# Kernel tuning notes

Measured on AMD Instinct MI355X. Metric: run time of the kernel, lower is better.

Reference implementation:

```python
import jax, jax.numpy as jnp
import numpy as np

CH = 512
NUM_GROUPS = 32
EPS = 1e-6

def _xavier(key, shape):
    fan_in, fan_out = shape[1], shape[0]
    limit = np.sqrt(6.0 / (fan_in + fan_out))
    return jax.random.uniform(key, shape, jnp.float32, -limit, limit)

def setup_inputs() -> dict:
    key = jax.random.key(0)
    ks = jax.random.split(key, 6)
    B, C, H, W = 32, CH, 32, 32
    x = jax.random.normal(ks[0], (B, C, H, W), jnp.float32)
    # 1x1 conv weights stored as [C_out, C_in]; biases zero (per initialize())
    wq = _xavier(ks[1], (C, C)); wk = _xavier(ks[2], (C, C))
    wv = _xavier(ks[3], (C, C)); wp = _xavier(ks[4], (C, C))
    bq = jnp.zeros((C,)); bk = jnp.zeros((C,)); bv = jnp.zeros((C,)); bp = jnp.zeros((C,))
    gn_w = jnp.ones((C,)); gn_b = jnp.zeros((C,))
    return {"x": x, "gn_w": gn_w, "gn_b": gn_b,
            "wq": wq, "bq": bq, "wk": wk, "bk": bk,
            "wv": wv, "bv": bv, "wp": wp, "bp": bp}

def _group_norm(x, w, b):
    B, C, H, W = x.shape
    g = NUM_GROUPS
    xg = x.reshape(B, g, C // g, H, W)
    mean = xg.mean(axis=(2, 3, 4), keepdims=True)
    var = xg.var(axis=(2, 3, 4), keepdims=True)
    xn = ((xg - mean) * jax.lax.rsqrt(var + EPS)).reshape(B, C, H, W)
    return xn * w[None, :, None, None] + b[None, :, None, None]

def reference(x, gn_w, gn_b, wq, bq, wk, bk, wv, bv, wp, bp):
    B, C, H, W = x.shape
    h = _group_norm(x, gn_w, gn_b)
    hf = h.reshape(B, C, H * W)  # [B, C, N]
    # 1x1 convs == per-pixel linear over channels
    q = jnp.einsum('oc,bcn->bno', wq, hf) + bq  # [B, N, C]
    k = jnp.einsum('oc,bcn->bon', wk, hf) + bk[None, :, None]  # [B, C, N]
    v = jnp.einsum('oc,bcn->bno', wv, hf) + bv  # [B, N, C]
    attn = jnp.einsum('bqc,bck->bqk', q, k) * (C ** -0.5)  # [B, N, N]
    attn = jax.nn.softmax(attn, axis=-1)
    out = jnp.einsum('bqk,bkc->bqc', attn, v)  # [B, N, C]
    out = jnp.einsum('oc,bnc->bon', wp, out) + bp[None, :, None]  # [B, C, N]
    return x + out.reshape(B, C, H, W)
```

## Files before the change

kernel.cpp:

```cpp
#include <hip/hip_runtime.h>


#define C_DIM 512
#define N_PIX 1024
#define BATCH 32
#define CPG 16
#define EPS 1e-6f
#define SCALE 0.044194173824159216f
#define ESTRIDE 66
#define ESTRU   72

typedef unsigned short u16;
typedef __attribute__((ext_vector_type(8))) short bf16x8;
typedef __attribute__((ext_vector_type(4))) float f32x4;
typedef __attribute__((ext_vector_type(2))) float f32x2;

static __device__ __forceinline__ float bf2f(u16 u) {
    union { unsigned int i; float f; } v; v.i = ((unsigned int)u) << 16; return v.f;
}
static __device__ __forceinline__ u16 f2bf(float f) {
    union { float f; unsigned int i; } v; v.f = f;
    unsigned int r = v.i + 0x7fffu + ((v.i >> 16) & 1u);
    return (u16)(r >> 16);
}

static __device__ __forceinline__ void gl_lds16(const u16* g, u16* l) {
    __builtin_amdgcn_global_load_lds(
        (const __attribute__((address_space(1))) unsigned int*)g,
        (__attribute__((address_space(3))) unsigned int*)l,
        16, 0, 0);
}

#define BAR()   __builtin_amdgcn_s_barrier()
#define SCHED() __builtin_amdgcn_sched_barrier(0x7)

__global__ __launch_bounds__(256) void wconv_kernel(
        const float* __restrict__ wq, const float* __restrict__ wk,
        const float* __restrict__ wv, const float* __restrict__ wp,
        u16* __restrict__ out) {
    int i = blockIdx.x * 256 + threadIdx.x;
    int mat = i >> 16;
    const float* src = (mat == 0) ? wq : (mat == 1) ? wk : (mat == 2) ? wv : wp;
    float4 v = ((const float4*)src)[i & 65535];
    ushort4 o;
    o.x = f2bf(v.x); o.y = f2bf(v.y); o.z = f2bf(v.z); o.w = f2bf(v.w);
    *(ushort4*)&out[(size_t)i * 4] = o;
}

__global__ __launch_bounds__(256) void gn_kernel(
        const float* __restrict__ x, const float* __restrict__ gw,
        const float* __restrict__ gb, u16* __restrict__ h) {
    int blk = blockIdx.x;
    int b = blk >> 5, g = blk & 31;
    size_t base = ((size_t)(b * C_DIM + g * CPG)) * N_PIX;
    const float4* xv = (const float4*)(x + base);
    int tid = threadIdx.x;

    float s = 0.f, sq = 0.f;
    for (int i = tid; i < (CPG * N_PIX) / 4; i += 256) {
        float4 v = xv[i];
        s  += v.x + v.y + v.z + v.w;
        sq += v.x * v.x + v.y * v.y + v.z * v.z + v.w * v.w;
    }
    __shared__ float rs[256], rq[256];
    rs[tid] = s; rq[tid] = sq;
    __syncthreads();
    for (int off = 128; off > 0; off >>= 1) {
        if (tid < off) { rs[tid] += rs[tid + off]; rq[tid] += rq[tid + off]; }
        __syncthreads();
    }
    float mean = rs[0] * (1.0f / (CPG * N_PIX));
    float var  = rq[0] * (1.0f / (CPG * N_PIX)) - mean * mean;
    float inv  = rsqrtf(var + EPS);

    __shared__ u16 Ls[CPG * N_PIX];
    for (int i = tid; i < (CPG * N_PIX) / 4; i += 256) {
        int c_local = i >> 8;
        int c = g * CPG + c_local;
        float sc = gw[c] * inv;
        float sh = gb[c] - mean * sc;
        float4 v = xv[i];
        ushort4 o;
        o.x = f2bf(v.x * sc + sh); o.y = f2bf(v.y * sc + sh);
        o.z = f2bf(v.z * sc + sh); o.w = f2bf(v.w * sc + sh);
        *(ushort4*)&Ls[c_local * N_PIX + (i & 255) * 4] = o;
    }
    __syncthreads();
    u16* hb = h + (size_t)b * N_PIX * C_DIM + g * CPG;
    for (int n = tid; n < N_PIX; n += 256) {
        unsigned int pk[8];
#pragma unroll
        for (int j = 0; j < 8; ++j) {
            unsigned int lo = Ls[(2 * j) * N_PIX + n];
            unsigned int hi = Ls[(2 * j + 1) * N_PIX + n];
            pk[j] = lo | (hi << 16);
        }
        uint4* dst = (uint4*)(hb + (size_t)n * C_DIM);
        dst[0] = make_uint4(pk[0], pk[1], pk[2], pk[3]);
        dst[1] = make_uint4(pk[4], pk[5], pk[6], pk[7]);
    }
}


#define MM(mq, nq) do { \
    _Pragma("unroll") \
    for (int t_ = 0; t_ < 4; ++t_) { \
        _Pragma("unroll") \
        for (int n_ = 0; n_ < 2; ++n_) { \
            _Pragma("unroll") \
            for (int ks_ = 0; ks_ < 2; ++ks_) \
                acc[(mq)*4 + t_][(nq)*2 + n_] = \
                    __builtin_amdgcn_mfma_f32_16x16x32_bf16( \
                        af[t_][ks_], bf[(nq)*2 + n_][ks_], \
                        acc[(mq)*4 + t_][(nq)*2 + n_], 0, 0, 0); \
        } \
    } \
} while (0)

template <int MODE>
__global__ __launch_bounds__(512, 2) void gemm_kernel(
        const u16* __restrict__ A, const u16* __restrict__ A2,
        const u16* __restrict__ B, const u16* __restrict__ B2,
        void* __restrict__ Cv, void* __restrict__ Cv2,
        const float* __restrict__ bias, const float* __restrict__ bias2,
        const float* __restrict__ xres, int K,
        int rsA, int rsB, int rsC,
        long long bsA, long long bsB, long long bsC) {
    int nx = gridDim.x, ny = gridDim.y;
    int nwg = nx * ny * gridDim.z;
    int flat = blockIdx.x + nx * (blockIdx.y + ny * blockIdx.z);
    int t = (flat & 7) * (nwg >> 3) + (flat >> 3);
    int bx = t % nx, by = (t / nx) % ny, bz = t / (nx * ny);

    int mat = 0, b = bz;
    const u16 *gA, *gB;
    void* out = Cv;
    const float* bi_p = bias;
    if (MODE == 0) {
        mat = bz & 1; b = bz >> 1;
        gA = A + (size_t)b * bsA + (size_t)by * 256 * rsA;
        gB = B + (size_t)mat * 262144 + (size_t)bx * 256 * rsB;
        out = mat ? Cv2 : Cv;
        bi_p = mat ? bias2 : bias;
    } else if (MODE == 2) {
        gA = A + (size_t)b * bsA + (size_t)by * 256 * rsA;
        gB = B + (size_t)b * bsB + (size_t)bx * 256 * rsB;
        out = (b >= 16) ? Cv2 : Cv;
    } else if (MODE == 3) {
        gA = ((b >= 16) ? A2 : A) + (size_t)(b & 15) * bsA + (size_t)by * 256 * rsA;
        gB = B + (size_t)b * bsB + (size_t)bx * 256 * rsB;
        out = (b >= 16) ? Cv2 : Cv;
    } else if (MODE == 4) {
        gA = A + (size_t)by * 256 * rsA;
        gB = ((b >= 16) ? B2 : B) + (size_t)(b & 15) * bsB + (size_t)bx * 256 * rsB;
    } else {
        gA = A + (size_t)by * 256 * rsA;
        gB = B + (size_t)b * bsB + (size_t)bx * 256 * rsB;
    }
    int cb = (MODE == 2 || MODE == 3) ? (b & 15) : b;

    __shared__ __align__(16) u16 smem[65536];

    int tid = threadIdx.x;
    int lane = tid & 63, wave = tid >> 6;
    int wm = wave >> 2, wn = wave & 3;
    int quad = lane >> 4, l15 = lane & 15, l7 = lane & 7;
    int srow = tid >> 3;
    int lg = (tid & 7) ^ (srow & 7);

    const int nk = K >> 6;
    const int nit = nk >> 1;

    auto STG = [&](int buf, int isB, int h, int kt) {
        const u16* g = isB ? gB : gA;
        int rs = isB ? rsB : rsA;
        const u16* src = g + (size_t)(h * 128 + srow) * rs + (size_t)kt * 64 + lg * 8;
        u16* dst = &smem[buf * 32768 + isB * 16384 + (h * 128 + srow) * 64 + (tid & 7) * 8];
        gl_lds16(src, dst);
        gl_lds16(src + (size_t)64 * rs, dst + 4096);
    };
    auto LDA = [&](int buf, int mq, int t_, int ks) -> bf16x8 {
        return *(const bf16x8*)&smem[buf * 32768 +
            (wm * 128 + mq * 64 + t_ * 16 + l15) * 64 + (((ks * 4 + quad) ^ l7) << 3)];
    };
    auto LDB = [&](int buf, int nt, int ks) -> bf16x8 {
        return *(const bf16x8*)&smem[buf * 32768 + 16384 +
            (wn * 64 + nt * 16 + l15) * 64 + (((ks * 4 + quad) ^ l7) << 3)];
    };

    f32x4 acc[8][4];
#pragma unroll
    for (int mt = 0; mt < 8; ++mt)
#pragma unroll
        for (int nt = 0; nt < 4; ++nt)
            acc[mt][nt] = (f32x4){0.f, 0.f, 0.f, 0.f};
    bf16x8 af[4][2], bf[4][2];

    STG(0, 1, 0, 0); STG(0, 1, 1, 0);
    STG(0, 0, 0, 0); STG(0, 0, 1, 0);
    STG(1, 1, 0, 1); STG(1, 1, 1, 1);
    asm volatile("s_waitcnt vmcnt(4)" ::: "memory");
    SCHED(); BAR(); SCHED();

    for (int it = 0; it < nit; ++it) {
        const bool s = (it + 1 < nit);
        const int k1 = 2 * it + 1, k2 = 2 * it + 2, k3 = 2 * it + 3;

#pragma unroll
        for (int t_ = 0; t_ < 4; ++t_)
#pragma unroll
            for (int ks = 0; ks < 2; ++ks) af[t_][ks] = LDA(0, 0, t_, ks);
#pragma unroll
        for (int n = 0; n < 2; ++n)
#pragma unroll
            for (int ks = 0; ks < 2; ++ks) bf[n][ks] = LDB(0, n, ks);
        STG(1, 0, 0, k1);
        SCHED(); BAR(); SCHED();
        __builtin_amdgcn_s_setprio(1); MM(0, 0); __builtin_amdgcn_s_setprio(0);
        SCHED(); BAR(); SCHED();

#pragma unroll
        for (int n = 2; n < 4; ++n)
#pragma unroll
            for (int ks = 0; ks < 2; ++ks) bf[n][ks] = LDB(0, n, ks);
        STG(1, 0, 1, k1);
        SCHED(); BAR(); SCHED();
        __builtin_amdgcn_s_setprio(1); MM(0, 1); __builtin_amdgcn_s_setprio(0);
        SCHED(); BAR(); SCHED();

#pragma unroll
        for (int t_ = 0; t_ < 4; ++t_)
#pragma unroll
            for (int ks = 0; ks < 2; ++ks) af[t_][ks] = LDA(0, 1, t_, ks);
        if (s) STG(0, 1, 0, k2);
        SCHED(); BAR(); SCHED();
        __builtin_amdgcn_s_setprio(1); MM(1, 1); __builtin_amdgcn_s_setprio(0);
        SCHED(); BAR(); SCHED();

        if (s) STG(0, 1, 1, k2);
        SCHED(); BAR(); SCHED();
        __builtin_amdgcn_s_setprio(1); MM(1, 0); __builtin_amdgcn_s_setprio(0);
        if (s) asm volatile("s_waitcnt vmcnt(4)" ::: "memory");
        else   asm volatile("s_waitcnt vmcnt(0)" ::: "memory");
        SCHED(); BAR(); SCHED();

#pragma unroll
        for (int t_ = 0; t_ < 4; ++t_)
#pragma unroll
            for (int ks = 0; ks < 2; ++ks) af[t_][ks] = LDA(1, 0, t_, ks);
#pragma unroll
        for (int n = 0; n < 2; ++n)
#pragma unroll
            for (int ks = 0; ks < 2; ++ks) bf[n][ks] = LDB(1, n, ks);
        if (s) STG(0, 0, 0, k2);
        SCHED(); BAR(); SCHED();
        __builtin_amdgcn_s_setprio(1); MM(0, 0); __builtin_amdgcn_s_setprio(0);
        SCHED(); BAR(); SCHED();

#pragma unroll
        for (int n = 2; n < 4; ++n)
#pragma unroll
            for (int ks = 0; ks < 2; ++ks) bf[n][ks] = LDB(1, n, ks);
        if (s) STG(0, 0, 1, k2);
        SCHED(); BAR(); SCHED();
        __builtin_amdgcn_s_setprio(1); MM(0, 1); __builtin_amdgcn_s_setprio(0);
        SCHED(); BAR(); SCHED();

#pragma unroll
        for (int t_ = 0; t_ < 4; ++t_)
#pragma unroll
            for (int ks = 0; ks < 2; ++ks) af[t_][ks] = LDA(1, 1, t_, ks);
        if (s) STG(1, 1, 0, k3);
        SCHED(); BAR(); SCHED();
        __builtin_amdgcn_s_setprio(1); MM(1, 1); __builtin_amdgcn_s_setprio(0);
        SCHED(); BAR(); SCHED();

        if (s) STG(1, 1, 1, k3);
        SCHED(); BAR(); SCHED();
        __builtin_amdgcn_s_setprio(1); MM(1, 0); __builtin_amdgcn_s_setprio(0);
        if (s) asm volatile("s_waitcnt vmcnt(4)" ::: "memory");
        SCHED(); BAR(); SCHED();
    }

    int colb = bx * 256 + wn * 64;
    int rowb = by * 256 + wm * 128;

    if (MODE == 4) {
        float* ebw = (float*)smem + wave * (16 * ESTRIDE);
        int er = lane >> 4;
        int ec4 = (lane & 15) * 4;
#pragma unroll
        for (int mt = 0; mt < 8; ++mt) {
#pragma unroll
            for (int nt = 0; nt < 4; ++nt) {
                f32x4 a = acc[mt][nt];
#pragma unroll
                for (int reg = 0; reg < 4; ++reg)
                    ebw[(quad * 4 + reg) * ESTRIDE + nt * 16 + l15] = a[reg];
            }
#pragma unroll
            for (int j = 0; j < 4; ++j) {
                int lr = er + 4 * j;
                f32x2 v0 = *(f32x2*)&ebw[lr * ESTRIDE + ec4];
                f32x2 v1 = *(f32x2*)&ebw[lr * ESTRIDE + ec4 + 2];
                int gr = rowb + mt * 16 + lr;
                int gc = colb + ec4;
                size_t cidx = (size_t)cb * bsC + (size_t)gr * rsC + gc;
                float bi = bi_p[gr];
                float4 xr = *(const float4*)&xres[cidx];
                float4 st = make_float4(v0.x + bi + xr.x, v0.y + bi + xr.y,
                                        v1.x + bi + xr.z, v1.y + bi + xr.w);
                *(float4*)&((float*)out)[cidx] = st;
            }
        }
    } else {
        u16* ebw = (u16*)smem + wave * (16 * ESTRU);
        int er = lane >> 3;
        int ec = (lane & 7) * 8;
        float bcol[4];
        if (MODE == 0) {
#pragma unroll
            for (int nt = 0; nt < 4; ++nt)
                bcol[nt] = bi_p[colb + nt * 16 + l15];
        }
#pragma unroll
        for (int mt = 0; mt < 8; ++mt) {
            float4 brow;
            if (MODE == 1)
                brow = *(const float4*)&bi_p[rowb + mt * 16 + quad * 4];
#pragma unroll
            for (int nt = 0; nt < 4; ++nt) {
                f32x4 a = acc[mt][nt];
#pragma unroll
                for (int reg = 0; reg < 4; ++reg) {
                    float fv = a[reg];
                    if (MODE == 0) fv += bcol[nt];
                    else if (MODE == 1) fv += ((const float*)&brow)[reg];
                    else if (MODE == 2) fv *= SCALE;
                    ebw[(quad * 4 + reg) * ESTRU + nt * 16 + l15] = f2bf(fv);
                }
            }
#pragma unroll
            for (int j = 0; j < 2; ++j) {
                int lr = er + 8 * j;
                bf16x8 vv = *(const bf16x8*)&ebw[lr * ESTRU + ec];
                int gr = rowb + mt * 16 + lr;
                size_t cidx = (size_t)cb * bsC + (size_t)gr * rsC + colb + ec;
                *(bf16x8*)&((u16*)out)[cidx] = vv;
            }
        }
    }
}

__global__ __launch_bounds__(256) void softmax_kernel(
        u16* __restrict__ S0, u16* __restrict__ S1) {
    int row = blockIdx.x;
    u16* base = (row & 16384) ? S1 : S0;
    u16* p = base + (size_t)(row & 16383) * N_PIX;
    int tid = threadIdx.x;
    ushort4 uv = *(ushort4*)&p[tid * 4];
    float4 v = make_float4(bf2f(uv.x), bf2f(uv.y), bf2f(uv.z), bf2f(uv.w));
    __shared__ float red[256];
    float m = fmaxf(fmaxf(v.x, v.y), fmaxf(v.z, v.w));
    red[tid] = m; __syncthreads();
    for (int off = 128; off > 0; off >>= 1) {
        if (tid < off) red[tid] = fmaxf(red[tid], red[tid + off]);
        __syncthreads();
    }
    float M = red[0];
    __syncthreads();
    float4 e;
    e.x = __expf(v.x - M); e.y = __expf(v.y - M);
    e.z = __expf(v.z - M); e.w = __expf(v.w - M);
    red[tid] = e.x + e.y + e.z + e.w; __syncthreads();
    for (int off = 128; off > 0; off >>= 1) {
        if (tid < off) red[tid] += red[tid + off];
        __syncthreads();
    }
    float inv = 1.0f / red[0];
    ushort4 st;
    st.x = f2bf(e.x * inv); st.y = f2bf(e.y * inv);
    st.z = f2bf(e.z * inv); st.w = f2bf(e.w * inv);
    *(ushort4*)&p[tid * 4] = st;
}

extern "C" void kernel_launch(void* const* d_in, const int* in_sizes, int n_in,
                              void* d_out, int out_size, void* d_ws, size_t ws_size,
                              hipStream_t stream) {
    const float* x    = (const float*)d_in[0];
    const float* gn_w = (const float*)d_in[1];
    const float* gn_b = (const float*)d_in[2];
    const float* wq   = (const float*)d_in[3];
    const float* bq   = (const float*)d_in[4];
    const float* wk   = (const float*)d_in[5];
    const float* bk   = (const float*)d_in[6];
    const float* wv   = (const float*)d_in[7];
    const float* bv   = (const float*)d_in[8];
    const float* wp   = (const float*)d_in[9];
    const float* bp   = (const float*)d_in[10];
    float* y = (float*)d_out;

    const size_t BCN = (size_t)BATCH * C_DIM * N_PIX;
    char* w = (char*)d_ws;
    u16* h  = (u16*)(w);
    u16* q  = (u16*)(w + 2 * BCN);
    u16* k  = (u16*)(w + 4 * BCN);
    u16* v  = (u16*)(w + 6 * BCN);
    u16* Or = (u16*)(w + 8 * BCN);
    u16* wb = (u16*)(w + 10 * BCN);
    u16* wvb = wb + 524288, *wpb = wb + 786432;
    u16* S0 = h;
    u16* S1 = Or;
    u16* O0 = q;
    u16* O1 = k;

    const long long BS = 524288;
    const long long SB = 1048576;

    wconv_kernel<<<1024, 256, 0, stream>>>(wq, wk, wv, wp, wb);
    gn_kernel<<<1024, 256, 0, stream>>>(x, gn_w, gn_b, h);

    gemm_kernel<0><<<dim3(2, 4, 64), 512, 0, stream>>>(
        h, nullptr, wb, nullptr, q, k, bq, bk, nullptr,
        512, 512, 512, 512, BS, 0, BS);
    gemm_kernel<1><<<dim3(4, 2, 32), 512, 0, stream>>>(
        wvb, nullptr, h, nullptr, v, nullptr, bv, nullptr, nullptr,
        512, 512, 512, 1024, 0, BS, BS);

    gemm_kernel<2><<<dim3(4, 4, 32), 512, 0, stream>>>(
        q, nullptr, k, nullptr, S0, S1, nullptr, nullptr, nullptr,
        512, 512, 512, 1024, BS, BS, SB);
    softmax_kernel<<<32 * 1024, 256, 0, stream>>>(S0, S1);
    gemm_kernel<3><<<dim3(2, 4, 32), 512, 0, stream>>>(
        S0, S1, v, nullptr, O0, O1, nullptr, nullptr, nullptr,
        1024, 1024, 1024, 512, SB, BS, BS);

    gemm_kernel<4><<<dim3(4, 2, 32), 512, 0, stream>>>(
        wpb, nullptr, O0, O1, y, nullptr, bp, nullptr, x,
        512, 512, 512, 1024, 0, BS, BS);
}
```

Measured before the change: 359.0 us.

## Persistent multi-tile GEMM with cross-tile prefetch, split groupnorm, warp-level softmax

```diff
diff --git a/kernel.cpp b/kernel.cpp
--- a/kernel.cpp
+++ b/kernel.cpp
@@ -34,70 +34,90 @@
 #define BAR()   __builtin_amdgcn_s_barrier()
 #define SCHED() __builtin_amdgcn_sched_barrier(0x7)
 
-__global__ __launch_bounds__(256) void wconv_kernel(
+__global__ __launch_bounds__(256) void prep_kernel(
         const float* __restrict__ wq, const float* __restrict__ wk,
         const float* __restrict__ wv, const float* __restrict__ wp,
-        u16* __restrict__ out) {
-    int i = blockIdx.x * 256 + threadIdx.x;
-    int mat = i >> 16;
-    const float* src = (mat == 0) ? wq : (mat == 1) ? wk : (mat == 2) ? wv : wp;
-    float4 v = ((const float4*)src)[i & 65535];
-    ushort4 o;
-    o.x = f2bf(v.x); o.y = f2bf(v.y); o.z = f2bf(v.z); o.w = f2bf(v.w);
-    *(ushort4*)&out[(size_t)i * 4] = o;
-}
-
-__global__ __launch_bounds__(256) void gn_kernel(
-        const float* __restrict__ x, const float* __restrict__ gw,
-        const float* __restrict__ gb, u16* __restrict__ h) {
+        u16* __restrict__ out, const float* __restrict__ x,
+        float* __restrict__ stats) {
     int blk = blockIdx.x;
+    if (blk < 1024) {
+        int i = blk * 256 + threadIdx.x;
+        int mat = i >> 16;
+        const float* src = (mat == 0) ? wq : (mat == 1) ? wk : (mat == 2) ? wv : wp;
+        float4 v = ((const float4*)src)[i & 65535];
+        ushort4 o;
+        o.x = f2bf(v.x); o.y = f2bf(v.y); o.z = f2bf(v.z); o.w = f2bf(v.w);
+        *(ushort4*)&out[(size_t)i * 4] = o;
+        return;
+    }
+    blk -= 1024;
     int b = blk >> 5, g = blk & 31;
-    size_t base = ((size_t)(b * C_DIM + g * CPG)) * N_PIX;
-    const float4* xv = (const float4*)(x + base);
+    const float4* xv = (const float4*)(x + ((size_t)(b * C_DIM + g * CPG)) * N_PIX);
     int tid = threadIdx.x;
-
     float s = 0.f, sq = 0.f;
+#pragma unroll 4
     for (int i = tid; i < (CPG * N_PIX) / 4; i += 256) {
         float4 v = xv[i];
         s  += v.x + v.y + v.z + v.w;
         sq += v.x * v.x + v.y * v.y + v.z * v.z + v.w * v.w;
     }
-    __shared__ float rs[256], rq[256];
-    rs[tid] = s; rq[tid] = sq;
+#pragma unroll
+    for (int m = 1; m < 64; m <<= 1) {
+        s += __shfl_xor(s, m);
+        sq += __shfl_xor(sq, m);
+    }
+    __shared__ float rs[4], rq[4];
+    int wv_ = tid >> 6;
+    if ((tid & 63) == 0) { rs[wv_] = s; rq[wv_] = sq; }
     __syncthreads();
-    for (int off = 128; off > 0; off >>= 1) {
-        if (tid < off) { rs[tid] += rs[tid + off]; rq[tid] += rq[tid + off]; }
-        __syncthreads();
-    }
-    float mean = rs[0] * (1.0f / (CPG * N_PIX));
-    float var  = rq[0] * (1.0f / (CPG * N_PIX)) - mean * mean;
-    float inv  = rsqrtf(var + EPS);
-
-    __shared__ u16 Ls[CPG * N_PIX];
-    for (int i = tid; i < (CPG * N_PIX) / 4; i += 256) {
-        int c_local = i >> 8;
-        int c = g * CPG + c_local;
+    if (tid == 0) {
+        float S = rs[0] + rs[1] + rs[2] + rs[3];
+        float Q = rq[0] + rq[1] + rq[2] + rq[3];
+        float mean = S * (1.0f / (CPG * N_PIX));
+        float var  = Q * (1.0f / (CPG * N_PIX)) - mean * mean;
+        stats[blk * 2] = mean;
+        stats[blk * 2 + 1] = rsqrtf(var + EPS);
+    }
+}
+
+__global__ __launch_bounds__(256) void gnt_kernel(
+        const float* __restrict__ x, const float* __restrict__ gw,
+        const float* __restrict__ gb, const float* __restrict__ stats,
+        u16* __restrict__ h) {
+    int blk = blockIdx.x;
+    int b = blk >> 4, nc = blk & 15;
+    int n0 = nc * 64;
+    __shared__ u16 T[64 * 520];
+    int tid = threadIdx.x;
+    int cq = tid >> 4;
+    int n4 = tid & 15;
+    const float* xb = x + (size_t)b * C_DIM * N_PIX + n0;
+#pragma unroll 4
+    for (int pass = 0; pass < 32; ++pass) {
+        int c = pass * 16 + cq;
+        int g = c >> 4;
+        float mean = stats[(b * 32 + g) * 2];
+        float inv  = stats[(b * 32 + g) * 2 + 1];
         float sc = gw[c] * inv;
         float sh = gb[c] - mean * sc;
-        float4 v = xv[i];
-        ushort4 o;
-        o.x = f2bf(v.x * sc + sh); o.y = f2bf(v.y * sc + sh);
-        o.z = f2bf(v.z * sc + sh); o.w = f2bf(v.w * sc + sh);
-        *(ushort4*)&Ls[c_local * N_PIX + (i & 255) * 4] = o;
+        float4 v = *(const float4*)(xb + (size_t)c * N_PIX + n4 * 4);
+        int nn = n4 * 4;
+        T[(nn + 0) * 520 + c] = f2bf(v.x * sc + sh);
+        T[(nn + 1) * 520 + c] = f2bf(v.y * sc + sh);
+        T[(nn + 2) * 520 + c] = f2bf(v.z * sc + sh);
+        T[(nn + 3) * 520 + c] = f2bf(v.w * sc + sh);
     }
     __syncthreads();
-    u16* hb = h + (size_t)b * N_PIX * C_DIM + g * CPG;
-    for (int n = tid; n < N_PIX; n += 256) {
-        unsigned int pk[8];
-#pragma unroll
-        for (int j = 0; j < 8; ++j) {
-            unsigned int lo = Ls[(2 * j) * N_PIX + n];
-            unsigned int hi = Ls[(2 * j + 1) * N_PIX + n];
-            pk[j] = lo | (hi << 16);
-        }
-        uint4* dst = (uint4*)(hb + (size_t)n * C_DIM);
-        dst[0] = make_uint4(pk[0], pk[1], pk[2], pk[3]);
-        dst[1] = make_uint4(pk[4], pk[5], pk[6], pk[7]);
+    u16* hb = h + ((size_t)b * N_PIX + n0) * C_DIM;
+    int rr = tid >> 5;
+    int cc = (tid & 31) * 16;
+#pragma unroll
+    for (int p = 0; p < 8; ++p) {
+        int n = p * 8 + rr;
+        bf16x8 v0 = *(const bf16x8*)&T[n * 520 + cc];
+        bf16x8 v1 = *(const bf16x8*)&T[n * 520 + cc + 8];
+        *(bf16x8*)&hb[(size_t)n * C_DIM + cc] = v0;
+        *(bf16x8*)&hb[(size_t)n * C_DIM + cc + 8] = v1;
     }
 }
 
@@ -117,7 +137,7 @@
     } \
 } while (0)
 
-template <int MODE>
+template <int MODE, int NT>
 __global__ __launch_bounds__(512, 2) void gemm_kernel(
         const u16* __restrict__ A, const u16* __restrict__ A2,
         const u16* __restrict__ B, const u16* __restrict__ B2,
@@ -125,39 +145,47 @@
         const float* __restrict__ bias, const float* __restrict__ bias2,
         const float* __restrict__ xres, int K,
         int rsA, int rsB, int rsC,
-        long long bsA, long long bsB, long long bsC) {
-    int nx = gridDim.x, ny = gridDim.y;
-    int nwg = nx * ny * gridDim.z;
-    int flat = blockIdx.x + nx * (blockIdx.y + ny * blockIdx.z);
-    int t = (flat & 7) * (nwg >> 3) + (flat >> 3);
-    int bx = t % nx, by = (t / nx) % ny, bz = t / (nx * ny);
-
-    int mat = 0, b = bz;
-    const u16 *gA, *gB;
-    void* out = Cv;
-    const float* bi_p = bias;
-    if (MODE == 0) {
-        mat = bz & 1; b = bz >> 1;
-        gA = A + (size_t)b * bsA + (size_t)by * 256 * rsA;
-        gB = B + (size_t)mat * 262144 + (size_t)bx * 256 * rsB;
-        out = mat ? Cv2 : Cv;
-        bi_p = mat ? bias2 : bias;
-    } else if (MODE == 2) {
-        gA = A + (size_t)b * bsA + (size_t)by * 256 * rsA;
-        gB = B + (size_t)b * bsB + (size_t)bx * 256 * rsB;
-        out = (b >= 16) ? Cv2 : Cv;
-    } else if (MODE == 3) {
-        gA = ((b >= 16) ? A2 : A) + (size_t)(b & 15) * bsA + (size_t)by * 256 * rsA;
-        gB = B + (size_t)b * bsB + (size_t)bx * 256 * rsB;
-        out = (b >= 16) ? Cv2 : Cv;
-    } else if (MODE == 4) {
-        gA = A + (size_t)by * 256 * rsA;
-        gB = ((b >= 16) ? B2 : B) + (size_t)(b & 15) * bsB + (size_t)bx * 256 * rsB;
-    } else {
-        gA = A + (size_t)by * 256 * rsA;
-        gB = B + (size_t)b * bsB + (size_t)bx * 256 * rsB;
-    }
-    int cb = (MODE == 2 || MODE == 3) ? (b & 15) : b;
+        long long bsA, long long bsB, long long bsC,
+        int nx, int ny) {
+    const int nwg = 256 * NT;
+
+    const u16* tgA[2]; const u16* tgB[2];
+    void* tout[2]; const float* tbi[2];
+    int tcb[2], tcolb[2], trowb[2];
+#pragma unroll
+    for (int tt = 0; tt < NT; ++tt) {
+        int flat = blockIdx.x + tt * 256;
+        int t = (flat & 7) * (nwg >> 3) + (flat >> 3);
+        int bx = t % nx, by = (t / nx) % ny, bz = t / (nx * ny);
+        int b = bz;
+        const u16 *gA, *gB;
+        void* out = Cv;
+        const float* bi = bias;
+        if (MODE == 0) {
+            int mat = bz & 1; b = bz >> 1;
+            gA = A + (size_t)b * bsA + (size_t)by * 256 * rsA;
+            gB = B + (size_t)mat * 262144 + (size_t)bx * 256 * rsB;
+            out = mat ? Cv2 : Cv;
+            bi = mat ? bias2 : bias;
+        } else if (MODE == 2) {
+            gA = A + (size_t)b * bsA + (size_t)by * 256 * rsA;
+            gB = B + (size_t)b * bsB + (size_t)bx * 256 * rsB;
+            out = (b >= 16) ? Cv2 : Cv;
+        } else if (MODE == 3) {
+            gA = ((b >= 16) ? A2 : A) + (size_t)(b & 15) * bsA + (size_t)by * 256 * rsA;
+            gB = B + (size_t)b * bsB + (size_t)bx * 256 * rsB;
+            out = (b >= 16) ? Cv2 : Cv;
+        } else if (MODE == 4) {
+            gA = A + (size_t)by * 256 * rsA;
+            gB = ((b >= 16) ? B2 : B) + (size_t)(b & 15) * bsB + (size_t)bx * 256 * rsB;
+        } else {
+            gA = A + (size_t)by * 256 * rsA;
+            gB = B + (size_t)b * bsB + (size_t)bx * 256 * rsB;
+        }
+        tgA[tt] = gA; tgB[tt] = gB; tout[tt] = out; tbi[tt] = bi;
+        tcb[tt] = (MODE == 2 || MODE == 3) ? (b & 15) : b;
+        tcolb[tt] = bx * 256; trowb[tt] = by * 256;
+    }
 
     __shared__ __align__(16) u16 smem[65536];
 
@@ -171,11 +199,9 @@
     const int nk = K >> 6;
     const int nit = nk >> 1;
 
-    auto STG = [&](int buf, int isB, int h, int kt) {
-        const u16* g = isB ? gB : gA;
-        int rs = isB ? rsB : rsA;
-        const u16* src = g + (size_t)(h * 128 + srow) * rs + (size_t)kt * 64 + lg * 8;
-        u16* dst = &smem[buf * 32768 + isB * 16384 + (h * 128 + srow) * 64 + (tid & 7) * 8];
+    auto STG = [&](const u16* g, int rs, int buf, int isB, int hh, int kt) {
+        const u16* src = g + (size_t)(hh * 128 + srow) * rs + (size_t)kt * 64 + lg * 8;
+        u16* dst = &smem[buf * 32768 + isB * 16384 + (hh * 128 + srow) * 64 + (tid & 7) * 8];
         gl_lds16(src, dst);
         gl_lds16(src + (size_t)64 * rs, dst + 4096);
     };
@@ -189,199 +215,228 @@
     };
 
     f32x4 acc[8][4];
-#pragma unroll
-    for (int mt = 0; mt < 8; ++mt)
-#pragma unroll
-        for (int nt = 0; nt < 4; ++nt)
-            acc[mt][nt] = (f32x4){0.f, 0.f, 0.f, 0.f};
     bf16x8 af[4][2], bf[4][2];
 
-    STG(0, 1, 0, 0); STG(0, 1, 1, 0);
-    STG(0, 0, 0, 0); STG(0, 0, 1, 0);
-    STG(1, 1, 0, 1); STG(1, 1, 1, 1);
-    asm volatile("s_waitcnt vmcnt(4)" ::: "memory");
-    SCHED(); BAR(); SCHED();
-
-    for (int it = 0; it < nit; ++it) {
-        const bool s = (it + 1 < nit);
-        const int k1 = 2 * it + 1, k2 = 2 * it + 2, k3 = 2 * it + 3;
-
-#pragma unroll
-        for (int t_ = 0; t_ < 4; ++t_)
-#pragma unroll
-            for (int ks = 0; ks < 2; ++ks) af[t_][ks] = LDA(0, 0, t_, ks);
-#pragma unroll
-        for (int n = 0; n < 2; ++n)
-#pragma unroll
-            for (int ks = 0; ks < 2; ++ks) bf[n][ks] = LDB(0, n, ks);
-        STG(1, 0, 0, k1);
-        SCHED(); BAR(); SCHED();
-        __builtin_amdgcn_s_setprio(1); MM(0, 0); __builtin_amdgcn_s_setprio(0);
-        SCHED(); BAR(); SCHED();
-
-#pragma unroll
-        for (int n = 2; n < 4; ++n)
-#pragma unroll
-            for (int ks = 0; ks < 2; ++ks) bf[n][ks] = LDB(0, n, ks);
-        STG(1, 0, 1, k1);
-        SCHED(); BAR(); SCHED();
-        __builtin_amdgcn_s_setprio(1); MM(0, 1); __builtin_amdgcn_s_setprio(0);
-        SCHED(); BAR(); SCHED();
-
-#pragma unroll
-        for (int t_ = 0; t_ < 4; ++t_)
-#pragma unroll
-            for (int ks = 0; ks < 2; ++ks) af[t_][ks] = LDA(0, 1, t_, ks);
-        if (s) STG(0, 1, 0, k2);
-        SCHED(); BAR(); SCHED();
-        __builtin_amdgcn_s_setprio(1); MM(1, 1); __builtin_amdgcn_s_setprio(0);
-        SCHED(); BAR(); SCHED();
-
-        if (s) STG(0, 1, 1, k2);
-        SCHED(); BAR(); SCHED();
-        __builtin_amdgcn_s_setprio(1); MM(1, 0); __builtin_amdgcn_s_setprio(0);
-        if (s) asm volatile("s_waitcnt vmcnt(4)" ::: "memory");
-        else   asm volatile("s_waitcnt vmcnt(0)" ::: "memory");
-        SCHED(); BAR(); SCHED();
-
-#pragma unroll
-        for (int t_ = 0; t_ < 4; ++t_)
-#pragma unroll
-            for (int ks = 0; ks < 2; ++ks) af[t_][ks] = LDA(1, 0, t_, ks);
-#pragma unroll
-        for (int n = 0; n < 2; ++n)
-#pragma unroll
-            for (int ks = 0; ks < 2; ++ks) bf[n][ks] = LDB(1, n, ks);
-        if (s) STG(0, 0, 0, k2);
-        SCHED(); BAR(); SCHED();
-        __builtin_amdgcn_s_setprio(1); MM(0, 0); __builtin_amdgcn_s_setprio(0);
-        SCHED(); BAR(); SCHED();
-
-#pragma unroll
-        for (int n = 2; n < 4; ++n)
-#pragma unroll
-            for (int ks = 0; ks < 2; ++ks) bf[n][ks] = LDB(1, n, ks);
-        if (s) STG(0, 0, 1, k2);
-        SCHED(); BAR(); SCHED();
-        __builtin_amdgcn_s_setprio(1); MM(0, 1); __builtin_amdgcn_s_setprio(0);
-        SCHED(); BAR(); SCHED();
-
-#pragma unroll
-        for (int t_ = 0; t_ < 4; ++t_)
-#pragma unroll
-            for (int ks = 0; ks < 2; ++ks) af[t_][ks] = LDA(1, 1, t_, ks);
-        if (s) STG(1, 1, 0, k3);
-        SCHED(); BAR(); SCHED();
-        __builtin_amdgcn_s_setprio(1); MM(1, 1); __builtin_amdgcn_s_setprio(0);
-        SCHED(); BAR(); SCHED();
-
-        if (s) STG(1, 1, 1, k3);
-        SCHED(); BAR(); SCHED();
-        __builtin_amdgcn_s_setprio(1); MM(1, 0); __builtin_amdgcn_s_setprio(0);
-        if (s) asm volatile("s_waitcnt vmcnt(4)" ::: "memory");
-        SCHED(); BAR(); SCHED();
-    }
-
-    int colb = bx * 256 + wn * 64;
-    int rowb = by * 256 + wm * 128;
-
-    if (MODE == 4) {
-        float* ebw = (float*)smem + wave * (16 * ESTRIDE);
-        int er = lane >> 4;
-        int ec4 = (lane & 15) * 4;
-#pragma unroll
-        for (int mt = 0; mt < 8; ++mt) {
-#pragma unroll
-            for (int nt = 0; nt < 4; ++nt) {
-                f32x4 a = acc[mt][nt];
-#pragma unroll
-                for (int reg = 0; reg < 4; ++reg)
-                    ebw[(quad * 4 + reg) * ESTRIDE + nt * 16 + l15] = a[reg];
+#pragma unroll
+    for (int tt = 0; tt < NT; ++tt) {
+        const bool hn = (tt + 1 < NT);
+        const u16* cA = tgA[tt];
+        const u16* cB = tgB[tt];
+        const u16* nA = tgA[hn ? tt + 1 : tt];
+        const u16* nB = tgB[hn ? tt + 1 : tt];
+
+        if (tt == 0) {
+            STG(cB, rsB, 0, 1, 0, 0); STG(cB, rsB, 0, 1, 1, 0);
+            STG(cA, rsA, 0, 0, 0, 0); STG(cA, rsA, 0, 0, 1, 0);
+            STG(cB, rsB, 1, 1, 0, 1); STG(cB, rsB, 1, 1, 1, 1);
+            asm volatile("s_waitcnt vmcnt(4)" ::: "memory");
+            SCHED(); BAR(); SCHED();
+        }
+
+#pragma unroll
+        for (int mt = 0; mt < 8; ++mt)
+#pragma unroll
+            for (int nt = 0; nt < 4; ++nt)
+                acc[mt][nt] = (f32x4){0.f, 0.f, 0.f, 0.f};
+
+        for (int it = 0; it < nit; ++it) {
+            const bool s = (it + 1 < nit);
+            const int k1 = 2 * it + 1, k2 = 2 * it + 2, k3 = 2 * it + 3;
+
+#pragma unroll
+            for (int t_ = 0; t_ < 4; ++t_)
+#pragma unroll
+                for (int ks = 0; ks < 2; ++ks) af[t_][ks] = LDA(0, 0, t_, ks);
+#pragma unroll
+            for (int n = 0; n < 2; ++n)
+#pragma unroll
+                for (int ks = 0; ks < 2; ++ks) bf[n][ks] = LDB(0, n, ks);
+            STG(cA, rsA, 1, 0, 0, k1);
+            SCHED(); BAR(); SCHED();
+            __builtin_amdgcn_s_setprio(1); MM(0, 0); __builtin_amdgcn_s_setprio(0);
+            SCHED(); BAR(); SCHED();
+
+#pragma unroll
+            for (int n = 2; n < 4; ++n)
+#pragma unroll
+                for (int ks = 0; ks < 2; ++ks) bf[n][ks] = LDB(0, n, ks);
+            STG(cA, rsA, 1, 0, 1, k1);
+            SCHED(); BAR(); SCHED();
+            __builtin_amdgcn_s_setprio(1); MM(0, 1); __builtin_amdgcn_s_setprio(0);
+            SCHED(); BAR(); SCHED();
+
+#pragma unroll
+            for (int t_ = 0; t_ < 4; ++t_)
+#pragma unroll
+                for (int ks = 0; ks < 2; ++ks) af[t_][ks] = LDA(0, 1, t_, ks);
+            if (s) STG(cB, rsB, 0, 1, 0, k2);
+            else if (hn) STG(nB, rsB, 0, 1, 0, 0);
+            SCHED(); BAR(); SCHED();
+            __builtin_amdgcn_s_setprio(1); MM(1, 1); __builtin_amdgcn_s_setprio(0);
+            SCHED(); BAR(); SCHED();
+
+            if (s) STG(cB, rsB, 0, 1, 1, k2);
+            else if (hn) STG(nB, rsB, 0, 1, 1, 0);
+            SCHED(); BAR(); SCHED();
+            __builtin_amdgcn_s_setprio(1); MM(1, 0); __builtin_amdgcn_s_setprio(0);
+            if (s || hn) asm volatile("s_waitcnt vmcnt(4)" ::: "memory");
+            else         asm volatile("s_waitcnt vmcnt(0)" ::: "memory");
+            SCHED(); BAR(); SCHED();
+
+#pragma unroll
+            for (int t_ = 0; t_ < 4; ++t_)
+#pragma unroll
+                for (int ks = 0; ks < 2; ++ks) af[t_][ks] = LDA(1, 0, t_, ks);
+#pragma unroll
+            for (int n = 0; n < 2; ++n)
+#pragma unroll
+                for (int ks = 0; ks < 2; ++ks) bf[n][ks] = LDB(1, n, ks);
+            if (s) STG(cA, rsA, 0, 0, 0, k2);
+            else if (hn) STG(nA, rsA, 0, 0, 0, 0);
+            SCHED(); BAR(); SCHED();
+            __builtin_amdgcn_s_setprio(1); MM(0, 0); __builtin_amdgcn_s_setprio(0);
+            SCHED(); BAR(); SCHED();
+
+#pragma unroll
+            for (int n = 2; n < 4; ++n)
+#pragma unroll
+                for (int ks = 0; ks < 2; ++ks) bf[n][ks] = LDB(1, n, ks);
+            if (s) STG(cA, rsA, 0, 0, 1, k2);
+            else if (hn) STG(nA, rsA, 0, 0, 1, 0);
+            SCHED(); BAR(); SCHED();
+            __builtin_amdgcn_s_setprio(1); MM(0, 1); __builtin_amdgcn_s_setprio(0);
+            SCHED(); BAR(); SCHED();
+
+#pragma unroll
+            for (int t_ = 0; t_ < 4; ++t_)
+#pragma unroll
+                for (int ks = 0; ks < 2; ++ks) af[t_][ks] = LDA(1, 1, t_, ks);
+            if (s) STG(cB, rsB, 1, 1, 0, k3);
+            else if (hn) STG(nB, rsB, 1, 1, 0, 1);
+            SCHED(); BAR(); SCHED();
+            __builtin_amdgcn_s_setprio(1); MM(1, 1); __builtin_amdgcn_s_setprio(0);
+            SCHED(); BAR(); SCHED();
+
+            if (s) STG(cB, rsB, 1, 1, 1, k3);
+            else if (hn) STG(nB, rsB, 1, 1, 1, 1);
+            SCHED(); BAR(); SCHED();
+            __builtin_amdgcn_s_setprio(1); MM(1, 0); __builtin_amdgcn_s_setprio(0);
+            if (s) asm volatile("s_waitcnt vmcnt(4)" ::: "memory");
+            SCHED(); BAR(); SCHED();
+        }
+
+        int colb = tcolb[tt] + wn * 64;
+        int rowb = trowb[tt] + wm * 128;
+        void* out = tout[tt];
+        const float* bi_p = tbi[tt];
+        int cb = tcb[tt];
+
+        if (MODE == 4) {
+            float* ebw = (float*)(smem + 32768) + wave * (16 * ESTRIDE);
+            int er = lane >> 4;
+            int ec4 = (lane & 15) * 4;
+#pragma unroll
+            for (int mt = 0; mt < 8; ++mt) {
+#pragma unroll
+                for (int nt = 0; nt < 4; ++nt) {
+                    f32x4 a = acc[mt][nt];
+#pragma unroll
+                    for (int reg = 0; reg < 4; ++reg)
+                        ebw[(quad * 4 + reg) * ESTRIDE + nt * 16 + l15] = a[reg];
+                }
+#pragma unroll
+                for (int j = 0; j < 4; ++j) {
+                    int lr = er + 4 * j;
+                    f32x2 v0 = *(f32x2*)&ebw[lr * ESTRIDE + ec4];
+                    f32x2 v1 = *(f32x2*)&ebw[lr * ESTRIDE + ec4 + 2];
+                    int gr = rowb + mt * 16 + lr;
+                    int gc = colb + ec4;
+                    size_t cidx = (size_t)cb * bsC + (size_t)gr * rsC + gc;
+                    float bi = bi_p[gr];
+                    float4 xr = *(const float4*)&xres[cidx];
+                    float4 st = make_float4(v0.x + bi + xr.x, v0.y + bi + xr.y,
+                                            v1.x + bi + xr.z, v1.y + bi + xr.w);
+                    *(float4*)&((float*)out)[cidx] = st;
+                }
             }
-#pragma unroll
-            for (int j = 0; j < 4; ++j) {
-                int lr = er + 4 * j;
-                f32x2 v0 = *(f32x2*)&ebw[lr * ESTRIDE + ec4];
-                f32x2 v1 = *(f32x2*)&ebw[lr * ESTRIDE + ec4 + 2];
-                int gr = rowb + mt * 16 + lr;
-                int gc = colb + ec4;
-                size_t cidx = (size_t)cb * bsC + (size_t)gr * rsC + gc;
-                float bi = bi_p[gr];
-                float4 xr = *(const float4*)&xres[cidx];
-                float4 st = make_float4(v0.x + bi + xr.x, v0.y + bi + xr.y,
-                                        v1.x + bi + xr.z, v1.y + bi + xr.w);
-                *(float4*)&((float*)out)[cidx] = st;
+        } else {
+            u16* ebw = (smem + 32768) + wave * (16 * ESTRU);
+            int er = lane >> 3;
+            int ec = (lane & 7) * 8;
+            float bcol[4];
+            if (MODE == 0) {
+#pragma unroll
+                for (int nt = 0; nt < 4; ++nt)
+                    bcol[nt] = bi_p[colb + nt * 16 + l15];
+            }
+#pragma unroll
+            for (int mt = 0; mt < 8; ++mt) {
+                float4 brow;
+                if (MODE == 1)
+                    brow = *(const float4*)&bi_p[rowb + mt * 16 + quad * 4];
+#pragma unroll
+                for (int nt = 0; nt < 4; ++nt) {
+                    f32x4 a = acc[mt][nt];
+#pragma unroll
+                    for (int reg = 0; reg < 4; ++reg) {
+                        float fv = a[reg];
+                        if (MODE == 0) fv += bcol[nt];
+                        else if (MODE == 1) fv += ((const float*)&brow)[reg];
+                        else if (MODE == 2) fv *= SCALE;
+                        ebw[(quad * 4 + reg) * ESTRU + nt * 16 + l15] = f2bf(fv);
+                    }
+                }
+#pragma unroll
+                for (int j = 0; j < 2; ++j) {
+                    int lr = er + 8 * j;
+                    bf16x8 vv = *(const bf16x8*)&ebw[lr * ESTRU + ec];
+                    int gr = rowb + mt * 16 + lr;
+                    size_t cidx = (size_t)cb * bsC + (size_t)gr * rsC + colb + ec;
+                    *(bf16x8*)&((u16*)out)[cidx] = vv;
+                }
             }
         }
-    } else {
-        u16* ebw = (u16*)smem + wave * (16 * ESTRU);
-        int er = lane >> 3;
-        int ec = (lane & 7) * 8;
-        float bcol[4];
-        if (MODE == 0) {
-#pragma unroll
-            for (int nt = 0; nt < 4; ++nt)
-                bcol[nt] = bi_p[colb + nt * 16 + l15];
-        }
-#pragma unroll
-        for (int mt = 0; mt < 8; ++mt) {
-            float4 brow;
-            if (MODE == 1)
-                brow = *(const float4*)&bi_p[rowb + mt * 16 + quad * 4];
-#pragma unroll
-            for (int nt = 0; nt < 4; ++nt) {
-                f32x4 a = acc[mt][nt];
-#pragma unroll
-                for (int reg = 0; reg < 4; ++reg) {
-                    float fv = a[reg];
-                    if (MODE == 0) fv += bcol[nt];
-                    else if (MODE == 1) fv += ((const float*)&brow)[reg];
-                    else if (MODE == 2) fv *= SCALE;
-                    ebw[(quad * 4 + reg) * ESTRU + nt * 16 + l15] = f2bf(fv);
-                }
-            }
-#pragma unroll
-            for (int j = 0; j < 2; ++j) {
-                int lr = er + 8 * j;
-                bf16x8 vv = *(const bf16x8*)&ebw[lr * ESTRU + ec];
-                int gr = rowb + mt * 16 + lr;
-                size_t cidx = (size_t)cb * bsC + (size_t)gr * rsC + colb + ec;
-                *(bf16x8*)&((u16*)out)[cidx] = vv;
-            }
+
+        if (hn) {
+            SCHED();
+            asm volatile("s_waitcnt vmcnt(20)" ::: "memory");
+            BAR(); SCHED();
         }
     }
 }
 
 __global__ __launch_bounds__(256) void softmax_kernel(
         u16* __restrict__ S0, u16* __restrict__ S1) {
-    int row = blockIdx.x;
-    u16* base = (row & 16384) ? S1 : S0;
-    u16* p = base + (size_t)(row & 16383) * N_PIX;
-    int tid = threadIdx.x;
-    ushort4 uv = *(ushort4*)&p[tid * 4];
-    float4 v = make_float4(bf2f(uv.x), bf2f(uv.y), bf2f(uv.z), bf2f(uv.w));
-    __shared__ float red[256];
-    float m = fmaxf(fmaxf(v.x, v.y), fmaxf(v.z, v.w));
-    red[tid] = m; __syncthreads();
-    for (int off = 128; off > 0; off >>= 1) {
-        if (tid < off) red[tid] = fmaxf(red[tid], red[tid + off]);
-        __syncthreads();
-    }
-    float M = red[0];
-    __syncthreads();
-    float4 e;
-    e.x = __expf(v.x - M); e.y = __expf(v.y - M);
-    e.z = __expf(v.z - M); e.w = __expf(v.w - M);
-    red[tid] = e.x + e.y + e.z + e.w; __syncthreads();
-    for (int off = 128; off > 0; off >>= 1) {
-        if (tid < off) red[tid] += red[tid + off];
-        __syncthreads();
-    }
-    float inv = 1.0f / red[0];
-    ushort4 st;
-    st.x = f2bf(e.x * inv); st.y = f2bf(e.y * inv);
-    st.z = f2bf(e.z * inv); st.w = f2bf(e.w * inv);
-    *(ushort4*)&p[tid * 4] = st;
+    int row = blockIdx.x * 4 + (threadIdx.x >> 6);
+    int lane = threadIdx.x & 63;
+    u16* p = ((row & 16384) ? S1 : S0) + (size_t)(row & 16383) * N_PIX + lane * 16;
+    bf16x8 u0 = *(const bf16x8*)p;
+    bf16x8 u1 = *(const bf16x8*)(p + 8);
+    float f[16];
+#pragma unroll
+    for (int i = 0; i < 8; ++i) {
+        f[i] = bf2f((u16)u0[i]);
+        f[8 + i] = bf2f((u16)u1[i]);
+    }
+    float m = f[0];
+#pragma unroll
+    for (int i = 1; i < 16; ++i) m = fmaxf(m, f[i]);
+#pragma unroll
+    for (int off = 1; off < 64; off <<= 1) m = fmaxf(m, __shfl_xor(m, off));
+    float s = 0.f;
+#pragma unroll
+    for (int i = 0; i < 16; ++i) { f[i] = __expf(f[i] - m); s += f[i]; }
+#pragma unroll
+    for (int off = 1; off < 64; off <<= 1) s += __shfl_xor(s, off);
+    float inv = 1.0f / s;
+    bf16x8 s0, s1;
+#pragma unroll
+    for (int i = 0; i < 8; ++i) {
+        s0[i] = (short)f2bf(f[i] * inv);
+        s1[i] = (short)f2bf(f[8 + i] * inv);
+    }
+    *(bf16x8*)p = s0;
+    *(bf16x8*)(p + 8) = s1;
 }
 
 extern "C" void kernel_launch(void* const* d_in, const int* in_sizes, int n_in,
@@ -409,6 +464,7 @@
     u16* Or = (u16*)(w + 8 * BCN);
     u16* wb = (u16*)(w + 10 * BCN);
     u16* wvb = wb + 524288, *wpb = wb + 786432;
+    float* stats = (float*)(w + 10 * BCN + 2 * 1024 * 1024);
     u16* S0 = h;
     u16* S1 = Or;
     u16* O0 = q;
@@ -417,25 +473,25 @@
     const long long BS = 524288;
     const long long SB = 1048576;
 
-    wconv_kernel<<<1024, 256, 0, stream>>>(wq, wk, wv, wp, wb);
-    gn_kernel<<<1024, 256, 0, stream>>>(x, gn_w, gn_b, h);
-
-    gemm_kernel<0><<<dim3(2, 4, 64), 512, 0, stream>>>(
+    prep_kernel<<<2048, 256, 0, stream>>>(wq, wk, wv, wp, wb, x, stats);
+    gnt_kernel<<<512, 256, 0, stream>>>(x, gn_w, gn_b, stats, h);
+
+    gemm_kernel<0, 2><<<256, 512, 0, stream>>>(
         h, nullptr, wb, nullptr, q, k, bq, bk, nullptr,
-        512, 512, 512, 512, BS, 0, BS);
-    gemm_kernel<1><<<dim3(4, 2, 32), 512, 0, stream>>>(
+        512, 512, 512, 512, BS, 0, BS, 2, 4);
+    gemm_kernel<1, 1><<<256, 512, 0, stream>>>(
         wvb, nullptr, h, nullptr, v, nullptr, bv, nullptr, nullptr,
-        512, 512, 512, 1024, 0, BS, BS);
-
-    gemm_kernel<2><<<dim3(4, 4, 32), 512, 0, stream>>>(
+        512, 512, 512, 1024, 0, BS, BS, 4, 2);
+
+    gemm_kernel<2, 2><<<256, 512, 0, stream>>>(
         q, nullptr, k, nullptr, S0, S1, nullptr, nullptr, nullptr,
-        512, 512, 512, 1024, BS, BS, SB);
-    softmax_kernel<<<32 * 1024, 256, 0, stream>>>(S0, S1);
-    gemm_kernel<3><<<dim3(2, 4, 32), 512, 0, stream>>>(
+        512, 512, 512, 1024, BS, BS, SB, 4, 4);
+    softmax_kernel<<<8192, 256, 0, stream>>>(S0, S1);
+    gemm_kernel<3, 1><<<256, 512, 0, stream>>>(
         S0, S1, v, nullptr, O0, O1, nullptr, nullptr, nullptr,
-        1024, 1024, 1024, 512, SB, BS, BS);
-
-    gemm_kernel<4><<<dim3(4, 2, 32), 512, 0, stream>>>(
+        1024, 1024, 1024, 512, SB, BS, BS, 2, 4);
+
+    gemm_kernel<4, 1><<<256, 512, 0, stream>>>(
         wpb, nullptr, O0, O1, y, nullptr, bp, nullptr, x,
-        512, 512, 512, 1024, 0, BS, BS);
-}
+        512, 512, 512, 1024, 0, BS, BS, 4, 2);
+}
```

After: 341.1 us. 1.05x faster.
